# Kernel optimization log

Measured on AMD Instinct MI355X. Metric: run time of the kernel, lower is better.

## Reference

```python
import jax, jax.numpy as jnp
import numpy as np
from jax import lax

EPS = 1e-8
DIL = 4  # 2**(dilation-1) with dilation=3


def prelu(x, a):
    return jnp.where(x >= 0, x, a * x)


def cln(x):
    # cumulative layer norm over (channels, causal time window); gamma=1, beta=0
    # x: [B, M, L]
    M = x.shape[1]
    L = x.shape[2]
    cnt = (M * jnp.arange(1, L + 1, dtype=x.dtype))  # [L]
    csum = jnp.cumsum(jnp.sum(x, axis=1), axis=-1)           # [B, L]
    csq = jnp.cumsum(jnp.sum(x * x, axis=1), axis=-1)        # [B, L]
    mean = csum / cnt                                         # [B, L]
    var = csq / cnt - mean * mean                             # [B, L]
    return (x - mean[:, None, :]) / jnp.sqrt(var[:, None, :] + EPS)


def depthwise_conv(x, dw, db):
    # x: [B, H, L]; dw: [H, 1, P]; grouped conv, groups=H, 'same' padding, dilation DIL
    y = lax.conv_general_dilated(
        x, dw,
        window_strides=(1,),
        padding='SAME',
        rhs_dilation=(DIL,),
        dimension_numbers=('NCH', 'OIH', 'NCH'),
        feature_group_count=x.shape[1],
    )
    return y + db[None, :, None]


def setup_inputs() -> dict:
    key = jax.random.key(0)
    ks = jax.random.split(key, 9)
    Bc, H, P, Sc = 128, 512, 3, 128
    bsz, L = 4, 8000
    return {
        'x': jax.random.normal(ks[0], (bsz, Bc, L), dtype=jnp.float32),
        'W1': jax.random.normal(ks[1], (H, Bc), dtype=jnp.float32) * 0.05,
        'b1': jax.random.normal(ks[2], (H,), dtype=jnp.float32) * 0.02,
        'dw': jax.random.normal(ks[3], (H, 1, P), dtype=jnp.float32) * 0.1,
        'db': jax.random.normal(ks[4], (H,), dtype=jnp.float32) * 0.02,
        'Wout': jax.random.normal(ks[5], (Bc, H), dtype=jnp.float32) * 0.05,
        'bout': jax.random.normal(ks[6], (Bc,), dtype=jnp.float32) * 0.02,
        'Wskip': jax.random.normal(ks[7], (Sc, H), dtype=jnp.float32) * 0.05,
        'bskip': jax.random.normal(ks[8], (Sc,), dtype=jnp.float32) * 0.02,
        'a1': jnp.full((1,), 0.25, dtype=jnp.float32),
        'a2': jnp.full((1,), 0.25, dtype=jnp.float32),
    }


def reference(x, W1, b1, dw, db, Wout, bout, Wskip, bskip, a1, a2):
    res_x = x
    h = jnp.einsum('bcl,hc->bhl', x, W1) + b1[None, :, None]   # conv1x1 (k=1)
    h = prelu(h, a1)
    h = cln(h)
    h = depthwise_conv(h, dw, db)
    h = prelu(h, a2)
    h = cln(h)
    out = jnp.einsum('bhl,ch->bcl', h, Wout) + bout[None, :, None] + res_x
    skip = jnp.einsum('bhl,sh->bsl', h, Wskip) + bskip[None, :, None]
    return (out, skip)
```

## Files before the change

kernel.cpp:

```cpp
#include <hip/hip_runtime.h>

typedef unsigned short u16;
typedef unsigned int u32;
typedef __attribute__((ext_vector_type(8))) short bf16x8;
typedef __attribute__((ext_vector_type(4))) float f32x4;

#define Bn 4
#define Cn 128
#define Hn 512
#define Ln 8000
#define EPSf 1e-8f

__device__ __forceinline__ float bf2f(u32 v) { return __uint_as_float(v << 16); }
__device__ __forceinline__ u32 f2bf(float f) {
  u32 u = __float_as_uint(f);
  return (u + 0x7fffu + ((u >> 16) & 1u)) >> 16;
}
__device__ __forceinline__ void gl16(const void* g, void* l) {
  __builtin_amdgcn_global_load_lds((const __attribute__((address_space(1))) u32*)g,
                                   (__attribute__((address_space(3))) u32*)l, 16, 0, 0);
}

__global__ void k0_prep(const float* __restrict__ W1, const float* __restrict__ Wout,
                        const float* __restrict__ Wskip,
                        u16* __restrict__ W1b, u16* __restrict__ Wcatb,
                        float* __restrict__ Wsum)
{
  const int bid = blockIdx.x, tid = threadIdx.x;
  if (bid < 64) {
    const int base = (bid * 256 + tid) * 4;
#pragma unroll
    for (int t = 0; t < 4; ++t) {
      int i = base + t;
      int h = i >> 7, k = i & 127;
      int dbyte = h * 256 + (((k * 2) ^ ((h & 7) << 4)));
      W1b[dbyte >> 1] = (u16)f2bf(W1[h * Cn + k]);
    }
  } else if (bid < 192) {
    const int base = ((bid - 64) * 256 + tid) * 4;
#pragma unroll
    for (int t = 0; t < 4; ++t) {
      int j = base + t;
      int kt = j >> 14, r = j & 16383, c = r >> 6, kk = r & 63;
      int k = kt * 64 + kk;
      float v = (c < Cn) ? Wout[c * Hn + k] : Wskip[(c - Cn) * Hn + k];
      int dbyte = kt * 32768 + c * 128 + (((kk * 2) ^ ((c & 7) << 4)));
      Wcatb[dbyte >> 1] = (u16)f2bf(v);
    }
  } else {
    const int c = tid;
    const float* Wp = (c < Cn) ? (Wout + (size_t)c * Hn) : (Wskip + (size_t)(c - Cn) * Hn);
    float s = 0.f;
    for (int k = 0; k < Hn; ++k) s += Wp[k];
    Wsum[c] = s;
  }
}

__global__ __launch_bounds__(256, 3)
void k1_fused(const float* __restrict__ x, const u16* __restrict__ W1b,
              const float* __restrict__ b1, const float* __restrict__ a1p,
              u16* __restrict__ hT, float* __restrict__ sum1, float* __restrict__ sumsq1)
{
  __shared__ char regA[32768];
  __shared__ char xs[16384];
  __shared__ float b1s[512];
  const int bidx = blockIdx.x;
  const int b = bidx / 125, l0 = (bidx % 125) * 64;
  const int tid = threadIdx.x, ln = tid & 63, w = tid >> 6;
  const int ln15 = ln & 15, lq = ln >> 4;

  {
    const char* xb = (const char*)x + ((size_t)b * Cn * Ln + l0) * 4;
#pragma unroll
    for (int i = 0; i < 8; ++i) {
      int chunk = w * 8 + i;
      gl16(xb + (size_t)(chunk * 4 + (ln >> 4)) * (Ln * 4) + (ln & 15) * 16,
           regA + chunk * 1024);
    }
  }
  b1s[tid] = b1[tid];
  b1s[tid + 256] = b1[tid + 256];
  __syncthreads();
#pragma unroll
  for (int p = 0; p < 4; ++p) {
    int u = tid + p * 256;
    int l = u & 63, ui = u >> 6;
    u32 pk[4];
#pragma unroll
    for (int pp = 0; pp < 4; ++pp) {
      int c0 = ui * 8 + pp * 2;
      float f0 = *(const float*)(regA + c0 * 256 + l * 4);
      float f1 = *(const float*)(regA + (c0 + 1) * 256 + l * 4);
      pk[pp] = f2bf(f0) | (f2bf(f1) << 16);
    }
    uint4 st; st.x = pk[0]; st.y = pk[1]; st.z = pk[2]; st.w = pk[3];
    *(uint4*)(xs + l * 256 + ((ui * 16) ^ ((l & 7) << 4))) = st;
  }

  const float a1v = a1p[0];
  float sAcc = 0.f, qAcc = 0.f;
  char* stg = regA;

  for (int s = 0; s < 4; ++s) {
    __syncthreads();
#pragma unroll
    for (int i = 0; i < 8; ++i) {
      int chunk = w * 8 + i;
      gl16((const char*)W1b + s * 32768 + chunk * 1024 + ln * 16, regA + chunk * 1024);
    }
    __syncthreads();

    f32x4 acc[8];
    const f32x4 z4 = {0.f, 0.f, 0.f, 0.f};
#pragma unroll
    for (int rf = 0; rf < 8; ++rf) acc[rf] = z4;
#pragma unroll
    for (int kf = 0; kf < 4; ++kf) {
      const int brow = w * 16 + ln15;
      bf16x8 bfr = *(const bf16x8*)(xs + brow * 256 +
                                    ((kf * 64 + lq * 16) ^ ((brow & 7) << 4)));
#pragma unroll
      for (int rf = 0; rf < 8; ++rf) {
        int arow = rf * 16 + ln15;
        bf16x8 afr = *(const bf16x8*)(regA + arow * 256 +
                                      ((kf * 64 + lq * 16) ^ ((arow & 7) << 4)));
        acc[rf] = __builtin_amdgcn_mfma_f32_16x16x32_bf16(afr, bfr, acc[rf], 0, 0, 0);
      }
    }
    __syncthreads();

#pragma unroll
    for (int rf = 0; rf < 8; ++rf) {
      int hb = s * 128 + rf * 16 + lq * 4;
      float v0 = acc[rf][0] + b1s[hb + 0]; v0 = v0 >= 0.f ? v0 : a1v * v0;
      float v1 = acc[rf][1] + b1s[hb + 1]; v1 = v1 >= 0.f ? v1 : a1v * v1;
      float v2 = acc[rf][2] + b1s[hb + 2]; v2 = v2 >= 0.f ? v2 : a1v * v2;
      float v3 = acc[rf][3] + b1s[hb + 3]; v3 = v3 >= 0.f ? v3 : a1v * v3;
      sAcc += v0 + v1 + v2 + v3;
      qAcc += v0 * v0 + v1 * v1 + v2 * v2 + v3 * v3;
      uint2 st2;
      st2.x = f2bf(v0) | (f2bf(v1) << 16);
      st2.y = f2bf(v2) | (f2bf(v3) << 16);
      *(uint2*)(stg + w * 4096 + ln15 * 256 +
                ((rf * 32 + lq * 8) ^ ((ln15 & 3) << 4))) = st2;
    }
#pragma unroll
    for (int p = 0; p < 4; ++p) {
      int lr = p * 4 + (ln >> 4);
      int j = ln & 15;
      uint4 v = *(const uint4*)(stg + w * 4096 + lr * 256 + ((j * 16) ^ ((lr & 3) << 4)));
      *(uint4*)((char*)hT + ((size_t)(b * Ln + l0 + w * 16 + lr)) * 1024 +
                s * 256 + j * 16) = v;
    }
  }
  sAcc += __shfl_xor(sAcc, 16); qAcc += __shfl_xor(qAcc, 16);
  sAcc += __shfl_xor(sAcc, 32); qAcc += __shfl_xor(qAcc, 32);
  if (lq == 0) {
    sum1[b * Ln + l0 + w * 16 + ln15] = sAcc;
    sumsq1[b * Ln + l0 + w * 16 + ln15] = qAcc;
  }
}

__global__ void k2_scan(const float* __restrict__ sum, const float* __restrict__ sumsq,
                        float* __restrict__ mean, float* __restrict__ rstd)
{
  const int b = blockIdx.x, tid = threadIdx.x;
  const int lane = tid & 63, w = tid >> 6;
  __shared__ float wts[4], wtq[4];
  float v[32], q[32];
  float ts = 0.f, tq = 0.f;
  const int base = tid * 32;
  const bool act = (tid < 250);
  if (act) {
#pragma unroll
    for (int i = 0; i < 8; ++i) {
      float4 a = *(const float4*)(sum + (size_t)b * Ln + base + i * 4);
      float4 c = *(const float4*)(sumsq + (size_t)b * Ln + base + i * 4);
      v[i * 4 + 0] = a.x; v[i * 4 + 1] = a.y; v[i * 4 + 2] = a.z; v[i * 4 + 3] = a.w;
      q[i * 4 + 0] = c.x; q[i * 4 + 1] = c.y; q[i * 4 + 2] = c.z; q[i * 4 + 3] = c.w;
    }
#pragma unroll
    for (int i = 0; i < 32; ++i) { ts += v[i]; tq += q[i]; }
  }
  float is = ts, iq = tq;
#pragma unroll
  for (int off = 1; off < 64; off <<= 1) {
    float a = __shfl_up(is, off);
    float c = __shfl_up(iq, off);
    if (lane >= off) { is += a; iq += c; }
  }
  float es = is - ts, eq = iq - tq;
  if (lane == 63) { wts[w] = is; wtq[w] = iq; }
  __syncthreads();
  for (int ww = 0; ww < w; ++ww) { es += wts[ww]; eq += wtq[ww]; }
  if (act) {
    float rs = es, rq = eq;
#pragma unroll
    for (int i = 0; i < 32; ++i) {
      rs += v[i]; rq += q[i];
      float cnt = 512.f * (float)(base + i + 1);
      float mn = rs / cnt;
      float var = fmaxf(rq / cnt - mn * mn, 0.f);
      v[i] = mn;
      q[i] = rsqrtf(var + EPSf);
    }
#pragma unroll
    for (int i = 0; i < 8; ++i) {
      float4 a; a.x = v[i*4+0]; a.y = v[i*4+1]; a.z = v[i*4+2]; a.w = v[i*4+3];
      float4 c; c.x = q[i*4+0]; c.y = q[i*4+1]; c.z = q[i*4+2]; c.w = q[i*4+3];
      *(float4*)(mean + (size_t)b * Ln + base + i * 4) = a;
      *(float4*)(rstd + (size_t)b * Ln + base + i * 4) = c;
    }
  }
}

__global__ __launch_bounds__(256, 2)
void k3_conv(const u16* __restrict__ hT, const float* __restrict__ mean1,
             const float* __restrict__ rstd1, const float* __restrict__ dw,
             const float* __restrict__ db, const float* __restrict__ a2p,
             u16* __restrict__ gT, float* __restrict__ sum2, float* __restrict__ sumsq2)
{
  __shared__ char hTs[73728];
  __shared__ float m1s[72], r1s[72];
  const int bidx = blockIdx.x;
  const int b = bidx / 125;
  const int l0 = (bidx % 125) * 64;
  const int tid = threadIdx.x;
  const int ln = tid & 63, w = tid >> 6;

  for (int i = 0; i < 18; ++i) {
    int chunk = w * 18 + i;
    int lr = l0 - 4 + chunk;
    int lc = lr < 0 ? 0 : (lr > Ln - 1 ? Ln - 1 : lr);
    gl16((const char*)hT + ((size_t)(b * Ln + lc)) * 1024 + ln * 16, hTs + chunk * 1024);
  }
  if (tid < 72) {
    int lr = l0 - 4 + tid;
    bool ok = (lr >= 0) && (lr < Ln);
    m1s[tid] = ok ? mean1[b * Ln + lr] : 0.f;
    r1s[tid] = ok ? rstd1[b * Ln + lr] : 0.f;
  }
  float d0[8], d1[8], d2[8], dbv[8];
#pragma unroll
  for (int e = 0; e < 8; ++e) {
    int hh = ln * 8 + e;
    d0[e] = dw[hh * 3 + 0]; d1[e] = dw[hh * 3 + 1]; d2[e] = dw[hh * 3 + 2];
    dbv[e] = db[hh];
  }
  const float a2v = a2p[0];
  __syncthreads();

  for (int it = 0; it < 16; ++it) {
    const int llo = w * 16 + it;
    const int l = l0 + llo;
    uint4 t0 = *reinterpret_cast<const uint4*>(hTs + (size_t)(llo) * 1024 + ln * 16);
    uint4 t1 = *reinterpret_cast<const uint4*>(hTs + (size_t)(llo + 4) * 1024 + ln * 16);
    uint4 t2 = *reinterpret_cast<const uint4*>(hTs + (size_t)(llo + 8) * 1024 + ln * 16);
    const float m0 = m1s[llo],     rr0 = r1s[llo];
    const float mC = m1s[llo + 4], rrC = r1s[llo + 4];
    const float m2v = m1s[llo + 8], rr2 = r1s[llo + 8];
    const u32* p0 = reinterpret_cast<const u32*>(&t0);
    const u32* p1 = reinterpret_cast<const u32*>(&t1);
    const u32* p2 = reinterpret_cast<const u32*>(&t2);
    float sv = 0.f, qv = 0.f;
    u32 outw[4];
#pragma unroll
    for (int pp = 0; pp < 4; ++pp) {
      float v01[2];
#pragma unroll
      for (int hi = 0; hi < 2; ++hi) {
        int e = pp * 2 + hi;
        u32 a0 = hi ? (p0[pp] >> 16) : (p0[pp] & 0xffffu);
        u32 a1b = hi ? (p1[pp] >> 16) : (p1[pp] & 0xffffu);
        u32 a2b = hi ? (p2[pp] >> 16) : (p2[pp] & 0xffffu);
        float nh0 = (bf2f(a0) - m0) * rr0;
        float nh1 = (bf2f(a1b) - mC) * rrC;
        float nh2 = (bf2f(a2b) - m2v) * rr2;
        float vv = fmaf(d0[e], nh0, fmaf(d1[e], nh1, fmaf(d2[e], nh2, dbv[e])));
        vv = vv >= 0.f ? vv : a2v * vv;
        sv += vv; qv += vv * vv;
        v01[hi] = vv;
      }
      outw[pp] = f2bf(v01[0]) | (f2bf(v01[1]) << 16);
    }
    uint4 st; st.x = outw[0]; st.y = outw[1]; st.z = outw[2]; st.w = outw[3];
    *reinterpret_cast<uint4*>((char*)gT + ((size_t)(b * Ln + l)) * 1024 +
                              (((ln * 16) ^ ((l & 7) << 4)))) = st;
#pragma unroll
    for (int off = 1; off < 64; off <<= 1) {
      sv += __shfl_xor(sv, off);
      qv += __shfl_xor(qv, off);
    }
    if (ln == 0) {
      sum2[b * Ln + l] = sv;
      sumsq2[b * Ln + l] = qv;
    }
  }
}

__global__ __launch_bounds__(256, 2)
void k5_gemm2(const u16* __restrict__ gT, const u16* __restrict__ Wcatb,
              const float* __restrict__ Wsum, const float* __restrict__ bout,
              const float* __restrict__ bskip, const float* __restrict__ mean2,
              const float* __restrict__ rstd2, const float* __restrict__ x,
              float* __restrict__ outp)
{
  __shared__ char Ab[2][32768];
  __shared__ char Bb[2][8192];
  const int bidx = blockIdx.x;
  const int b = bidx / 125;
  const int l0 = (bidx % 125) * 64;
  const int tid = threadIdx.x;
  const int ln = tid & 63, w = tid >> 6;
  const int ln15 = ln & 15, lq = ln >> 4;

  auto stage = [&](int kt, int bi) {
#pragma unroll
    for (int j = 0; j < 2; ++j) {
      int chunk = w * 2 + j;
      int lrow = chunk * 8 + (ln >> 3);
      int pos = (ln & 7) * 16;
      gl16((const char*)gT + ((size_t)(b * Ln + l0 + lrow)) * 1024 + kt * 128 + pos,
           Bb[bi] + chunk * 1024);
    }
    const char* Asrc = (const char*)Wcatb + kt * 32768;
#pragma unroll
    for (int i = 0; i < 8; ++i) {
      int chunk = w * 8 + i;
      gl16(Asrc + chunk * 1024 + ln * 16, Ab[bi] + chunk * 1024);
    }
  };

  f32x4 acc[4][4];
  const f32x4 z4 = {0.f, 0.f, 0.f, 0.f};
#pragma unroll
  for (int i = 0; i < 4; ++i)
#pragma unroll
    for (int j = 0; j < 4; ++j) acc[i][j] = z4;

  const int c0w = w * 64;
  stage(0, 0);
  __syncthreads();
  for (int kt = 0; kt < 8; ++kt) {
    const int cur = kt & 1;
    if (kt < 7) stage(kt + 1, cur ^ 1);
    const char* Ac = Ab[cur];
    const char* Bc = Bb[cur];
#pragma unroll
    for (int ks = 0; ks < 2; ++ks) {
      bf16x8 bfr[4];
#pragma unroll
      for (int cf = 0; cf < 4; ++cf) {
        int brow = cf * 16 + ln15;
        int off = ((ks * 64 + lq * 16) ^ ((brow & 7) << 4));
        bfr[cf] = *reinterpret_cast<const bf16x8*>(Bc + brow * 128 + off);
      }
#pragma unroll
      for (int rf = 0; rf < 4; ++rf) {
        int arow = c0w + rf * 16 + ln15;
        int aoff = ((ks * 64 + lq * 16) ^ ((arow & 7) << 4));
        bf16x8 afr = *reinterpret_cast<const bf16x8*>(Ac + arow * 128 + aoff);
#pragma unroll
        for (int cf = 0; cf < 4; ++cf)
          acc[rf][cf] = __builtin_amdgcn_mfma_f32_16x16x32_bf16(afr, bfr[cf], acc[rf][cf], 0, 0, 0);
      }
    }
    __syncthreads();
  }

  float wsr[4][4], bir[4][4];
#pragma unroll
  for (int rf = 0; rf < 4; ++rf)
#pragma unroll
    for (int r = 0; r < 4; ++r) {
      int c = c0w + rf * 16 + lq * 4 + r;
      wsr[rf][r] = Wsum[c];
      bir[rf][r] = (c < Cn) ? bout[c] : bskip[c - Cn];
    }
  const size_t OUTOFF = (size_t)Bn * Cn * Ln;
  char* stg = &Ab[0][0];
#pragma unroll
  for (int p = 0; p < 2; ++p) {
    if (p) __syncthreads();
#pragma unroll
    for (int cc = 0; cc < 2; ++cc) {
      const int cf = p * 2 + cc;
      const int ll = cc * 16 + ln15;
      const int l = l0 + cf * 16 + ln15;
      const float m2 = mean2[b * Ln + l];
      const float r2 = rstd2[b * Ln + l];
#pragma unroll
      for (int rf = 0; rf < 4; ++rf) {
#pragma unroll
        for (int r = 0; r < 4; ++r) {
          int c = c0w + rf * 16 + lq * 4 + r;
          float o = r2 * (acc[rf][cf][r] - m2 * wsr[rf][r]) + bir[rf][r];
          *(float*)(stg + c * 128 + ((((ll >> 2) ^ (c & 7)) << 4)) + (ll & 3) * 4) = o;
        }
      }
    }
    __syncthreads();
#pragma unroll
    for (int pp = 0; pp < 8; ++pp) {
      int i = pp * 256 + tid;
      int c = i >> 3, j = i & 7;
      float4 v = *(const float4*)(stg + c * 128 + (((j ^ (c & 7)) << 4)));
      int lcol = l0 + p * 32 + j * 4;
      if (c < Cn) {
        float4 xv = *(const float4*)(x + ((size_t)(b * Cn + c)) * Ln + lcol);
        v.x += xv.x; v.y += xv.y; v.z += xv.z; v.w += xv.w;
        *(float4*)(outp + ((size_t)(b * Cn + c)) * Ln + lcol) = v;
      } else {
        *(float4*)(outp + OUTOFF + ((size_t)(b * Cn + c - Cn)) * Ln + lcol) = v;
      }
    }
  }
}

extern "C" void kernel_launch(void* const* d_in, const int* in_sizes, int n_in,
                              void* d_out, int out_size, void* d_ws, size_t ws_size,
                              hipStream_t stream)
{
  const float* x     = (const float*)d_in[0];
  const float* W1    = (const float*)d_in[1];
  const float* b1    = (const float*)d_in[2];
  const float* dw    = (const float*)d_in[3];
  const float* db    = (const float*)d_in[4];
  const float* Wout  = (const float*)d_in[5];
  const float* bout  = (const float*)d_in[6];
  const float* Wskip = (const float*)d_in[7];
  const float* bskip = (const float*)d_in[8];
  const float* a1    = (const float*)d_in[9];
  const float* a2    = (const float*)d_in[10];
  float* outp = (float*)d_out;

  char* ws = (char*)d_ws;
  u16* hT     = (u16*)(ws);
  u16* gT     = (u16*)(ws + 32768000);
  u16* W1b    = (u16*)(ws + 65536000);
  u16* Wcatb  = (u16*)(ws + 65667072);
  float* Wsum   = (float*)(ws + 65929216);
  float* sum1   = (float*)(ws + 65930240);
  float* sumsq1 = (float*)(ws + 66058240);
  float* mean1  = (float*)(ws + 66186240);
  float* rstd1  = (float*)(ws + 66314240);
  float* sum2   = (float*)(ws + 66442240);
  float* sumsq2 = (float*)(ws + 66570240);
  float* mean2  = (float*)(ws + 66698240);
  float* rstd2  = (float*)(ws + 66826240);
  (void)in_sizes; (void)n_in; (void)out_size; (void)ws_size;

  hipLaunchKernelGGL(k0_prep, dim3(193), dim3(256), 0, stream,
                     W1, Wout, Wskip, W1b, Wcatb, Wsum);
  hipLaunchKernelGGL(k1_fused, dim3(Bn * 125), dim3(256), 0, stream,
                     x, W1b, b1, a1, hT, sum1, sumsq1);
  hipLaunchKernelGGL(k2_scan, dim3(Bn), dim3(256), 0, stream,
                     sum1, sumsq1, mean1, rstd1);
  hipLaunchKernelGGL(k3_conv, dim3(Bn * 125), dim3(256), 0, stream,
                     hT, mean1, rstd1, dw, db, a2, gT, sum2, sumsq2);
  hipLaunchKernelGGL(k2_scan, dim3(Bn), dim3(256), 0, stream,
                     sum2, sumsq2, mean2, rstd2);
  hipLaunchKernelGGL(k5_gemm2, dim3(Bn * 125), dim3(256), 0, stream,
                     gT, Wcatb, Wsum, bout, bskip, mean2, rstd2, x, outp);
}
```

Measured before the change: 94.23 us.

## Fuse cumulative-norm scans into consumers and read weights directly from global

```diff
diff --git a/kernel.cpp b/kernel.cpp
--- a/kernel.cpp
+++ b/kernel.cpp
@@ -28,30 +28,31 @@
 {
   const int bid = blockIdx.x, tid = threadIdx.x;
   if (bid < 64) {
-    const int base = (bid * 256 + tid) * 4;
-#pragma unroll
-    for (int t = 0; t < 4; ++t) {
-      int i = base + t;
-      int h = i >> 7, k = i & 127;
-      int dbyte = h * 256 + (((k * 2) ^ ((h & 7) << 4)));
-      W1b[dbyte >> 1] = (u16)f2bf(W1[h * Cn + k]);
-    }
+    const int i = (bid * 256 + tid) * 4;
+    float4 v = *(const float4*)(W1 + i);
+    u32 p0 = f2bf(v.x) | (f2bf(v.y) << 16);
+    u32 p1 = f2bf(v.z) | (f2bf(v.w) << 16);
+    uint2 st; st.x = p0; st.y = p1;
+    *(uint2*)(W1b + i) = st;
   } else if (bid < 192) {
-    const int base = ((bid - 64) * 256 + tid) * 4;
-#pragma unroll
-    for (int t = 0; t < 4; ++t) {
-      int j = base + t;
-      int kt = j >> 14, r = j & 16383, c = r >> 6, kk = r & 63;
-      int k = kt * 64 + kk;
-      float v = (c < Cn) ? Wout[c * Hn + k] : Wskip[(c - Cn) * Hn + k];
-      int dbyte = kt * 32768 + c * 128 + (((kk * 2) ^ ((c & 7) << 4)));
-      Wcatb[dbyte >> 1] = (u16)f2bf(v);
-    }
+    const int j = ((bid - 64) * 256 + tid) * 4;
+    const int c = j >> 9, k = j & 511;
+    const float* src = (c < Cn) ? (Wout + (size_t)c * Hn + k)
+                                : (Wskip + (size_t)(c - Cn) * Hn + k);
+    float4 v = *(const float4*)src;
+    u32 p0 = f2bf(v.x) | (f2bf(v.y) << 16);
+    u32 p1 = f2bf(v.z) | (f2bf(v.w) << 16);
+    uint2 st; st.x = p0; st.y = p1;
+    *(uint2*)(Wcatb + j) = st;
   } else {
     const int c = tid;
-    const float* Wp = (c < Cn) ? (Wout + (size_t)c * Hn) : (Wskip + (size_t)(c - Cn) * Hn);
+    const float4* Wp = (const float4*)((c < Cn) ? (Wout + (size_t)c * Hn)
+                                                : (Wskip + (size_t)(c - Cn) * Hn));
     float s = 0.f;
-    for (int k = 0; k < Hn; ++k) s += Wp[k];
+    for (int k = 0; k < 128; ++k) {
+      float4 v = Wp[k];
+      s += v.x + v.y + v.z + v.w;
+    }
     Wsum[c] = s;
   }
 }
@@ -94,22 +95,16 @@
       pk[pp] = f2bf(f0) | (f2bf(f1) << 16);
     }
     uint4 st; st.x = pk[0]; st.y = pk[1]; st.z = pk[2]; st.w = pk[3];
+    *(uint4*)(xs + l * 256 + ((ui * 16) ^ ((l & 7) << 4)));
     *(uint4*)(xs + l * 256 + ((ui * 16) ^ ((l & 7) << 4))) = st;
   }
+  __syncthreads();
 
   const float a1v = a1p[0];
   float sAcc = 0.f, qAcc = 0.f;
   char* stg = regA;
 
   for (int s = 0; s < 4; ++s) {
-    __syncthreads();
-#pragma unroll
-    for (int i = 0; i < 8; ++i) {
-      int chunk = w * 8 + i;
-      gl16((const char*)W1b + s * 32768 + chunk * 1024 + ln * 16, regA + chunk * 1024);
-    }
-    __syncthreads();
-
     f32x4 acc[8];
     const f32x4 z4 = {0.f, 0.f, 0.f, 0.f};
 #pragma unroll
@@ -121,14 +116,11 @@
                                     ((kf * 64 + lq * 16) ^ ((brow & 7) << 4)));
 #pragma unroll
       for (int rf = 0; rf < 8; ++rf) {
-        int arow = rf * 16 + ln15;
-        bf16x8 afr = *(const bf16x8*)(regA + arow * 256 +
-                                      ((kf * 64 + lq * 16) ^ ((arow & 7) << 4)));
+        int arow = s * 128 + rf * 16 + ln15;
+        bf16x8 afr = *(const bf16x8*)((const char*)W1b + arow * 256 + kf * 64 + lq * 16);
         acc[rf] = __builtin_amdgcn_mfma_f32_16x16x32_bf16(afr, bfr, acc[rf], 0, 0, 0);
       }
     }
-    __syncthreads();
-
 #pragma unroll
     for (int rf = 0; rf < 8; ++rf) {
       int hb = s * 128 + rf * 16 + lq * 4;
@@ -161,72 +153,22 @@
   }
 }
 
-__global__ void k2_scan(const float* __restrict__ sum, const float* __restrict__ sumsq,
-                        float* __restrict__ mean, float* __restrict__ rstd)
-{
-  const int b = blockIdx.x, tid = threadIdx.x;
-  const int lane = tid & 63, w = tid >> 6;
-  __shared__ float wts[4], wtq[4];
-  float v[32], q[32];
-  float ts = 0.f, tq = 0.f;
-  const int base = tid * 32;
-  const bool act = (tid < 250);
-  if (act) {
-#pragma unroll
-    for (int i = 0; i < 8; ++i) {
-      float4 a = *(const float4*)(sum + (size_t)b * Ln + base + i * 4);
-      float4 c = *(const float4*)(sumsq + (size_t)b * Ln + base + i * 4);
-      v[i * 4 + 0] = a.x; v[i * 4 + 1] = a.y; v[i * 4 + 2] = a.z; v[i * 4 + 3] = a.w;
-      q[i * 4 + 0] = c.x; q[i * 4 + 1] = c.y; q[i * 4 + 2] = c.z; q[i * 4 + 3] = c.w;
-    }
-#pragma unroll
-    for (int i = 0; i < 32; ++i) { ts += v[i]; tq += q[i]; }
-  }
-  float is = ts, iq = tq;
-#pragma unroll
-  for (int off = 1; off < 64; off <<= 1) {
-    float a = __shfl_up(is, off);
-    float c = __shfl_up(iq, off);
-    if (lane >= off) { is += a; iq += c; }
-  }
-  float es = is - ts, eq = iq - tq;
-  if (lane == 63) { wts[w] = is; wtq[w] = iq; }
-  __syncthreads();
-  for (int ww = 0; ww < w; ++ww) { es += wts[ww]; eq += wtq[ww]; }
-  if (act) {
-    float rs = es, rq = eq;
-#pragma unroll
-    for (int i = 0; i < 32; ++i) {
-      rs += v[i]; rq += q[i];
-      float cnt = 512.f * (float)(base + i + 1);
-      float mn = rs / cnt;
-      float var = fmaxf(rq / cnt - mn * mn, 0.f);
-      v[i] = mn;
-      q[i] = rsqrtf(var + EPSf);
-    }
-#pragma unroll
-    for (int i = 0; i < 8; ++i) {
-      float4 a; a.x = v[i*4+0]; a.y = v[i*4+1]; a.z = v[i*4+2]; a.w = v[i*4+3];
-      float4 c; c.x = q[i*4+0]; c.y = q[i*4+1]; c.z = q[i*4+2]; c.w = q[i*4+3];
-      *(float4*)(mean + (size_t)b * Ln + base + i * 4) = a;
-      *(float4*)(rstd + (size_t)b * Ln + base + i * 4) = c;
-    }
-  }
-}
-
 __global__ __launch_bounds__(256, 2)
-void k3_conv(const u16* __restrict__ hT, const float* __restrict__ mean1,
-             const float* __restrict__ rstd1, const float* __restrict__ dw,
+void k3_conv(const u16* __restrict__ hT, const float* __restrict__ sum1,
+             const float* __restrict__ sumsq1, const float* __restrict__ dw,
              const float* __restrict__ db, const float* __restrict__ a2p,
              u16* __restrict__ gT, float* __restrict__ sum2, float* __restrict__ sumsq2)
 {
   __shared__ char hTs[73728];
   __shared__ float m1s[72], r1s[72];
+  __shared__ float msc[128], rsc[128];
+  __shared__ float wts[4], wtq[4];
   const int bidx = blockIdx.x;
   const int b = bidx / 125;
   const int l0 = (bidx % 125) * 64;
   const int tid = threadIdx.x;
   const int ln = tid & 63, w = tid >> 6;
+  const int lane = ln;
 
   for (int i = 0; i < 18; ++i) {
     int chunk = w * 18 + i;
@@ -234,11 +176,54 @@
     int lc = lr < 0 ? 0 : (lr > Ln - 1 ? Ln - 1 : lr);
     gl16((const char*)hT + ((size_t)(b * Ln + lc)) * 1024 + ln * 16, hTs + chunk * 1024);
   }
+
+  const int sb = (l0 >= 4) ? (((l0 - 4) >> 5) << 5) : 0;
+  {
+    float v[32], q[32];
+    float ts = 0.f, tq = 0.f;
+    const int base = tid * 32;
+    const bool act = (tid < 250);
+    if (act) {
+#pragma unroll
+      for (int i = 0; i < 8; ++i) {
+        float4 a = *(const float4*)(sum1 + (size_t)b * Ln + base + i * 4);
+        float4 c = *(const float4*)(sumsq1 + (size_t)b * Ln + base + i * 4);
+        v[i * 4 + 0] = a.x; v[i * 4 + 1] = a.y; v[i * 4 + 2] = a.z; v[i * 4 + 3] = a.w;
+        q[i * 4 + 0] = c.x; q[i * 4 + 1] = c.y; q[i * 4 + 2] = c.z; q[i * 4 + 3] = c.w;
+      }
+#pragma unroll
+      for (int i = 0; i < 32; ++i) { ts += v[i]; tq += q[i]; }
+    }
+    float is = ts, iq = tq;
+#pragma unroll
+    for (int off = 1; off < 64; off <<= 1) {
+      float a = __shfl_up(is, off);
+      float c = __shfl_up(iq, off);
+      if (lane >= off) { is += a; iq += c; }
+    }
+    if (lane == 63) { wts[w] = is; wtq[w] = iq; }
+    __syncthreads();
+    float es = is - ts, eq = iq - tq;
+    for (int ww = 0; ww < w; ++ww) { es += wts[ww]; eq += wtq[ww]; }
+    if (act && (base + 32 > sb) && (base < sb + 128)) {
+      float rs = es, rq = eq;
+#pragma unroll
+      for (int i = 0; i < 32; ++i) {
+        rs += v[i]; rq += q[i];
+        float cnt = 512.f * (float)(base + i + 1);
+        float mn = rs / cnt;
+        float var = fmaxf(rq / cnt - mn * mn, 0.f);
+        msc[base + i - sb] = mn;
+        rsc[base + i - sb] = rsqrtf(var + EPSf);
+      }
+    }
+    __syncthreads();
+  }
   if (tid < 72) {
     int lr = l0 - 4 + tid;
     bool ok = (lr >= 0) && (lr < Ln);
-    m1s[tid] = ok ? mean1[b * Ln + lr] : 0.f;
-    r1s[tid] = ok ? rstd1[b * Ln + lr] : 0.f;
+    m1s[tid] = ok ? msc[lr - sb] : 0.f;
+    r1s[tid] = ok ? rsc[lr - sb] : 0.f;
   }
   float d0[8], d1[8], d2[8], dbv[8];
 #pragma unroll
@@ -298,38 +283,81 @@
   }
 }
 
-__global__ __launch_bounds__(256, 2)
+__global__ __launch_bounds__(256, 3)
 void k5_gemm2(const u16* __restrict__ gT, const u16* __restrict__ Wcatb,
               const float* __restrict__ Wsum, const float* __restrict__ bout,
-              const float* __restrict__ bskip, const float* __restrict__ mean2,
-              const float* __restrict__ rstd2, const float* __restrict__ x,
+              const float* __restrict__ bskip, const float* __restrict__ sum2,
+              const float* __restrict__ sumsq2, const float* __restrict__ x,
               float* __restrict__ outp)
 {
-  __shared__ char Ab[2][32768];
-  __shared__ char Bb[2][8192];
+  __shared__ char mem[32768];
+  __shared__ float m2s[64], r2s[64];
+  __shared__ float wts[4], wtq[4];
   const int bidx = blockIdx.x;
   const int b = bidx / 125;
   const int l0 = (bidx % 125) * 64;
   const int tid = threadIdx.x;
   const int ln = tid & 63, w = tid >> 6;
   const int ln15 = ln & 15, lq = ln >> 4;
-
-  auto stage = [&](int kt, int bi) {
+  const int lane = ln;
+
+  char* Bb0 = mem;
+  char* Bb1 = mem + 8192;
+
+  auto stageB = [&](int kt, char* dst) {
 #pragma unroll
     for (int j = 0; j < 2; ++j) {
       int chunk = w * 2 + j;
       int lrow = chunk * 8 + (ln >> 3);
       int pos = (ln & 7) * 16;
       gl16((const char*)gT + ((size_t)(b * Ln + l0 + lrow)) * 1024 + kt * 128 + pos,
-           Bb[bi] + chunk * 1024);
-    }
-    const char* Asrc = (const char*)Wcatb + kt * 32768;
-#pragma unroll
-    for (int i = 0; i < 8; ++i) {
-      int chunk = w * 8 + i;
-      gl16(Asrc + chunk * 1024 + ln * 16, Ab[bi] + chunk * 1024);
+           dst + chunk * 1024);
     }
   };
+
+  stageB(0, Bb0);
+
+  {
+    float v[32], q[32];
+    float ts = 0.f, tq = 0.f;
+    const int base = tid * 32;
+    const bool act = (tid < 250);
+    if (act) {
+#pragma unroll
+      for (int i = 0; i < 8; ++i) {
+        float4 a = *(const float4*)(sum2 + (size_t)b * Ln + base + i * 4);
+        float4 c = *(const float4*)(sumsq2 + (size_t)b * Ln + base + i * 4);
+        v[i * 4 + 0] = a.x; v[i * 4 + 1] = a.y; v[i * 4 + 2] = a.z; v[i * 4 + 3] = a.w;
+        q[i * 4 + 0] = c.x; q[i * 4 + 1] = c.y; q[i * 4 + 2] = c.z; q[i * 4 + 3] = c.w;
+      }
+#pragma unroll
+      for (int i = 0; i < 32; ++i) { ts += v[i]; tq += q[i]; }
+    }
+    float is = ts, iq = tq;
+#pragma unroll
+    for (int off = 1; off < 64; off <<= 1) {
+      float a = __shfl_up(is, off);
+      float c = __shfl_up(iq, off);
+      if (lane >= off) { is += a; iq += c; }
+    }
+    if (lane == 63) { wts[w] = is; wtq[w] = iq; }
+    __syncthreads();
+    float es = is - ts, eq = iq - tq;
+    for (int ww = 0; ww < w; ++ww) { es += wts[ww]; eq += wtq[ww]; }
+    if (act && (base + 32 > l0) && (base < l0 + 64)) {
+      float rs = es, rq = eq;
+#pragma unroll
+      for (int i = 0; i < 32; ++i) {
+        rs += v[i]; rq += q[i];
+        float cnt = 512.f * (float)(base + i + 1);
+        float mn = rs / cnt;
+        float var = fmaxf(rq / cnt - mn * mn, 0.f);
+        m2s[base + i - l0] = mn;
+        r2s[base + i - l0] = rsqrtf(var + EPSf);
+      }
+    }
+    __syncthreads();
+  }
 
   f32x4 acc[4][4];
   const f32x4 z4 = {0.f, 0.f, 0.f, 0.f};
@@ -339,13 +367,9 @@
     for (int j = 0; j < 4; ++j) acc[i][j] = z4;
 
   const int c0w = w * 64;
-  stage(0, 0);
-  __syncthreads();
   for (int kt = 0; kt < 8; ++kt) {
-    const int cur = kt & 1;
-    if (kt < 7) stage(kt + 1, cur ^ 1);
-    const char* Ac = Ab[cur];
-    const char* Bc = Bb[cur];
+    char* Bc = (kt & 1) ? Bb1 : Bb0;
+    if (kt < 7) stageB(kt + 1, (kt & 1) ? Bb0 : Bb1);
 #pragma unroll
     for (int ks = 0; ks < 2; ++ks) {
       bf16x8 bfr[4];
@@ -358,8 +382,8 @@
 #pragma unroll
       for (int rf = 0; rf < 4; ++rf) {
         int arow = c0w + rf * 16 + ln15;
-        int aoff = ((ks * 64 + lq * 16) ^ ((arow & 7) << 4));
-        bf16x8 afr = *reinterpret_cast<const bf16x8*>(Ac + arow * 128 + aoff);
+        bf16x8 afr = *(const bf16x8*)((const char*)Wcatb + (size_t)arow * 1024 +
+                                      kt * 128 + ks * 64 + lq * 16);
 #pragma unroll
         for (int cf = 0; cf < 4; ++cf)
           acc[rf][cf] = __builtin_amdgcn_mfma_f32_16x16x32_bf16(afr, bfr[cf], acc[rf][cf], 0, 0, 0);
@@ -378,7 +402,7 @@
       bir[rf][r] = (c < Cn) ? bout[c] : bskip[c - Cn];
     }
   const size_t OUTOFF = (size_t)Bn * Cn * Ln;
-  char* stg = &Ab[0][0];
+  char* stg = mem;
 #pragma unroll
   for (int p = 0; p < 2; ++p) {
     if (p) __syncthreads();
@@ -386,9 +410,9 @@
     for (int cc = 0; cc < 2; ++cc) {
       const int cf = p * 2 + cc;
       const int ll = cc * 16 + ln15;
-      const int l = l0 + cf * 16 + ln15;
-      const float m2 = mean2[b * Ln + l];
-      const float r2 = rstd2[b * Ln + l];
+      const int li = cf * 16 + ln15;
+      const float m2 = m2s[li];
+      const float r2 = r2s[li];
 #pragma unroll
       for (int rf = 0; rf < 4; ++rf) {
 #pragma unroll
@@ -442,24 +466,16 @@
   float* Wsum   = (float*)(ws + 65929216);
   float* sum1   = (float*)(ws + 65930240);
   float* sumsq1 = (float*)(ws + 66058240);
-  float* mean1  = (float*)(ws + 66186240);
-  float* rstd1  = (float*)(ws + 66314240);
   float* sum2   = (float*)(ws + 66442240);
   float* sumsq2 = (float*)(ws + 66570240);
-  float* mean2  = (float*)(ws + 66698240);
-  float* rstd2  = (float*)(ws + 66826240);
   (void)in_sizes; (void)n_in; (void)out_size; (void)ws_size;
 
   hipLaunchKernelGGL(k0_prep, dim3(193), dim3(256), 0, stream,
                      W1, Wout, Wskip, W1b, Wcatb, Wsum);
   hipLaunchKernelGGL(k1_fused, dim3(Bn * 125), dim3(256), 0, stream,
                      x, W1b, b1, a1, hT, sum1, sumsq1);
-  hipLaunchKernelGGL(k2_scan, dim3(Bn), dim3(256), 0, stream,
-                     sum1, sumsq1, mean1, rstd1);
   hipLaunchKernelGGL(k3_conv, dim3(Bn * 125), dim3(256), 0, stream,
-                     hT, mean1, rstd1, dw, db, a2, gT, sum2, sumsq2);
-  hipLaunchKernelGGL(k2_scan, dim3(Bn), dim3(256), 0, stream,
-                     sum2, sumsq2, mean2, rstd2);
+                     hT, sum1, sumsq1, dw, db, a2, gT, sum2, sumsq2);
   hipLaunchKernelGGL(k5_gemm2, dim3(Bn * 125), dim3(256), 0, stream,
-                     gT, Wcatb, Wsum, bout, bskip, mean2, rstd2, x, outp);
-}
+                     gT, Wcatb, Wsum, bout, bskip, sum2, sumsq2, x, outp);
+}
```

Measured after the change: 118.1 us. 25.3% more time.
